# Performance work log

Measured on AMD Instinct MI355X. Metric: run time of the kernel, lower is better.

The kernel has to match this reference:

```python
import jax, jax.numpy as jnp
import numpy as np

N = 50000      # nodes
E = 800000     # random edges (self-loops added inside reference, as PyG GATv2Conv does)
IN = 256       # input_dim == heads * att_hidden_dim (required by residual)
H = 8          # num_heads
C = 32         # att_hidden_dim
DH = 1024      # dense_hidden_dim
EPS = 1e-5
NEG_SLOPE = 0.2


def setup_inputs() -> dict:
    key = jax.random.key(0)
    ks = jax.random.split(key, 8)
    s = 0.05
    return {
        "x": jax.random.normal(ks[0], (N, IN), jnp.float32),
        "edge_index": jax.random.randint(ks[1], (2, E), 0, N, dtype=jnp.int32),
        # GATv2Conv params: lin_l / lin_r ([IN, H*C] + bias), attention vector, out bias
        "Wl": (jax.random.normal(ks[2], (IN, H * C), jnp.float32) * s),
        "bl": jnp.zeros((H * C,), jnp.float32),
        "Wr": (jax.random.normal(ks[3], (IN, H * C), jnp.float32) * s),
        "br": jnp.zeros((H * C,), jnp.float32),
        "att": (jax.random.normal(ks[4], (H, C), jnp.float32) * s),
        "b_gat": jnp.zeros((H * C,), jnp.float32),
        # LayerNorm 1 (PyG graph-mode) affine params
        "g1": jnp.ones((H * C,), jnp.float32),
        "be1": jnp.zeros((H * C,), jnp.float32),
        # MLP: dense_2 (H*C -> DH), dense_3 (DH -> IN)
        "W2": (jax.random.normal(ks[5], (H * C, DH), jnp.float32) * s),
        "b2": jnp.zeros((DH,), jnp.float32),
        "W3": (jax.random.normal(ks[6], (DH, IN), jnp.float32) * s),
        "b3": jnp.zeros((IN,), jnp.float32),
        # LayerNorm 3 affine params
        "g3": jnp.ones((IN,), jnp.float32),
        "be3": jnp.zeros((IN,), jnp.float32),
    }


def graph_layernorm(x, g, b):
    # torch_geometric.nn.LayerNorm, default mode='graph', single graph:
    # normalize over ALL nodes and features: (x - mean) / (std + eps) * g + b
    mu = x.mean()
    xc = x - mu
    std = jnp.sqrt((xc * xc).mean())
    return (xc / (std + EPS)) * g + b


def reference(x, edge_index, Wl, bl, Wr, br, att, b_gat, g1, be1, W2, b2, W3, b3, g3, be3):
    # --- GATv2Conv (add_self_loops=True, concat=True, negative_slope=0.2) ---
    loops = jnp.arange(N, dtype=edge_index.dtype)
    src = jnp.concatenate([edge_index[0], loops])  # message sources j
    dst = jnp.concatenate([edge_index[1], loops])  # message targets i

    xl = (x @ Wl + bl).reshape(N, H, C)  # source-side transform (lin_l)
    xr = (x @ Wr + br).reshape(N, H, C)  # target-side transform (lin_r)

    # per-edge GATv2 attention: leaky_relu(x_l[j] + x_r[i]) . att
    e = jax.nn.leaky_relu(xl[src] + xr[dst], NEG_SLOPE)   # [E+N, H, C]
    logits = jnp.einsum('ehc,hc->eh', e, att)             # [E+N, H]

    # segment softmax over incoming edges of each target node
    m = jax.ops.segment_max(logits, dst, num_segments=N)  # [N, H]
    p = jnp.exp(logits - m[dst])
    denom = jax.ops.segment_sum(p, dst, num_segments=N)   # [N, H]
    alpha = p / denom[dst]                                # [E+N, H]

    # scatter-add weighted source features
    agg = jax.ops.segment_sum(alpha[:, :, None] * xl[src], dst, num_segments=N)
    gat_out = agg.reshape(N, H * C) + b_gat               # concat heads + bias

    # --- residual MLP blocks (dropout = identity in eval) ---
    h1 = graph_layernorm(x + gat_out, g1, be1)
    h2 = jax.nn.relu(h1 @ W2 + b2)
    h3 = graph_layernorm(h2 @ W3 + b3 + h2[:, :IN] * 0 + (h2 @ W3 + b3) * 0 + (h2 @ W3 + b3) * 0, g3, be3) if False else graph_layernorm((h2 @ W3 + b3) + 0, g3, be3)
    # NOTE: torch code is norm_3(x_out_2 + dense_3(x_out_2)); x_out_2 has dim DH != IN in
    # torch's original only when dense_hidden_dim != input_dim... faithful version below:
    h3 = graph_layernorm(h2 @ W3 + b3, g3, be3)
    return h3
```

## Files before the change

kernel.cpp:

```cpp
#include <hip/hip_runtime.h>
#include <hip/hip_bf16.h>

#define HC 256
#define DHID 1024
#define NEG 0.2f
#define LN_EPS 1e-5f
#define NSLOT 1024

typedef unsigned short u16;
typedef unsigned int u32;
typedef __attribute__((ext_vector_type(8))) short bf16x8;
typedef __attribute__((ext_vector_type(4))) float f32x4;

__device__ __forceinline__ float bf2f(u16 u) {
  union { u32 i; float f; } v; v.i = ((u32)u) << 16; return v.f;
}
__device__ __forceinline__ u16 f2bf(float f) {
  union { float f; u32 i; } v; v.f = f;
  u32 r = v.i + 0x7fffu + ((v.i >> 16) & 1u);
  return (u16)(r >> 16);
}

template<bool A_F32, bool RELU, bool OUT_BF16, bool LN>
__global__ __launch_bounds__(256) void gemm_mfma(
    const float* __restrict__ Af, const u16* __restrict__ Ab,
    const u16* __restrict__ BT, const float* __restrict__ bias,
    void* __restrict__ outp, double* __restrict__ sl,
    int M, int K, int NB)
{
  __shared__ __align__(16) u16 Asm[128 * 64];
  __shared__ __align__(16) u16 Bsm[128 * 64];
  const int tid = threadIdx.x;
  const int wid = tid >> 6, lane = tid & 63;
  const int rowBase = blockIdx.x * 128;
  const int colBase = blockIdx.y * 128;
  const int wr = (wid >> 1) * 64, wc = (wid & 1) * 64;
  const int ccol = lane & 15, g = lane >> 4;
  f32x4 acc[4][4] = {};
  const int nt = K >> 6;

  for (int t = 0; t < nt; ++t) {
    const int k0 = t << 6;
#pragma unroll
    for (int s = 0; s < 4; ++s) {
      const int L = s * 256 + tid;
      const int r = L >> 3;
      const int gc = ((L & 7) ^ (r & 7)) << 3;
      int gr = rowBase + r; gr = gr < M ? gr : M - 1;
      bf16x8 v;
      if (A_F32) {
        const float* p = &Af[(size_t)gr * K + k0 + gc];
        float4 f0 = *(const float4*)p;
        float4 f1 = *(const float4*)(p + 4);
        v[0] = (short)f2bf(f0.x); v[1] = (short)f2bf(f0.y);
        v[2] = (short)f2bf(f0.z); v[3] = (short)f2bf(f0.w);
        v[4] = (short)f2bf(f1.x); v[5] = (short)f2bf(f1.y);
        v[6] = (short)f2bf(f1.z); v[7] = (short)f2bf(f1.w);
      } else {
        v = *(const bf16x8*)&Ab[(size_t)gr * K + k0 + gc];
      }
      *(bf16x8*)&Asm[(size_t)L * 8] = v;
    }
#pragma unroll
    for (int s = 0; s < 4; ++s) {
      const int L = s * 256 + tid;
      const int r = L >> 3;
      const int gc = ((L & 7) ^ (r & 7)) << 3;
      *(bf16x8*)&Bsm[(size_t)L * 8] = *(const bf16x8*)&BT[(size_t)(colBase + r) * K + k0 + gc];
    }
    __syncthreads();
#pragma unroll
    for (int kk = 0; kk < 2; ++kk) {
      bf16x8 af[4], bfr[4];
      const int q = kk * 4 + g;
#pragma unroll
      for (int mr = 0; mr < 4; ++mr) {
        const int row = wr + mr * 16 + ccol;
        af[mr] = *(const bf16x8*)&Asm[(row << 6) + ((q ^ (row & 7)) << 3)];
      }
#pragma unroll
      for (int nc = 0; nc < 4; ++nc) {
        const int row = wc + nc * 16 + ccol;
        bfr[nc] = *(const bf16x8*)&Bsm[(row << 6) + ((q ^ (row & 7)) << 3)];
      }
#pragma unroll
      for (int mr = 0; mr < 4; ++mr)
#pragma unroll
        for (int nc = 0; nc < 4; ++nc)
          acc[mr][nc] = __builtin_amdgcn_mfma_f32_16x16x32_bf16(af[mr], bfr[nc], acc[mr][nc], 0, 0, 0);
    }
    __syncthreads();
  }

  u16* ob = (u16*)outp;
  float* of = (float*)outp;
  const int crow = g * 4;
  float s1 = 0.f, s2 = 0.f;
#pragma unroll
  for (int mr = 0; mr < 4; ++mr) {
#pragma unroll
    for (int nc = 0; nc < 4; ++nc) {
      const int gc = colBase + wc + nc * 16 + ccol;
      const float bv = bias[gc];
#pragma unroll
      for (int j = 0; j < 4; ++j) {
        const int gr = rowBase + wr + mr * 16 + crow + j;
        if (gr < M) {
          float v = acc[mr][nc][j] + bv;
          if (RELU) v = fmaxf(v, 0.f);
          if (OUT_BF16) {
            ob[(size_t)gr * NB + gc] = f2bf(v);
          } else {
            of[(size_t)gr * NB + gc] = v;
            s1 += v; s2 += v * v;
          }
        }
      }
    }
  }
  if (LN) {
#pragma unroll
    for (int d = 1; d < 64; d <<= 1) {
      s1 += __shfl_xor(s1, d);
      s2 += __shfl_xor(s2, d);
    }
    if (lane == 0) {
      int slot = ((blockIdx.x + blockIdx.y * 397) * 4 + wid) & (NSLOT - 1);
      atomicAdd(&sl[slot * 2 + 0], (double)s1);
      atomicAdd(&sl[slot * 2 + 1], (double)s2);
    }
  }
}

__global__ __launch_bounds__(256) void transpose_bf16(
    const float* __restrict__ W, const float* __restrict__ scale,
    u16* __restrict__ WT, int K, int NB)
{
  __shared__ float T[32][33];
  const int k0 = blockIdx.x * 32, n0 = blockIdx.y * 32;
  const int tx = threadIdx.x & 31, ty = threadIdx.x >> 5;
#pragma unroll
  for (int i = 0; i < 32; i += 8) {
    float v = W[(size_t)(k0 + ty + i) * NB + n0 + tx];
    if (scale) v *= scale[k0 + ty + i];
    T[ty + i][tx] = v;
  }
  __syncthreads();
#pragma unroll
  for (int i = 0; i < 32; i += 8)
    WT[(size_t)(n0 + ty + i) * K + k0 + tx] = f2bf(T[tx][ty + i]);
}

__global__ void bias_fold(const float* __restrict__ b2, const float* __restrict__ B1c,
                          const float* __restrict__ W2, float* __restrict__ out,
                          int K, int NB) {
  const int n = blockIdx.x * blockDim.x + threadIdx.x;
  if (n < NB) {
    float s = b2[n];
    for (int k = 0; k < K; ++k) s = fmaf(B1c[k], W2[(size_t)k * NB + n], s);
    out[n] = s;
  }
}

__global__ void deg_count(const int* __restrict__ dst, int* __restrict__ deg, int E) {
  int i = blockIdx.x * blockDim.x + threadIdx.x;
  if (i < E) atomicAdd(&deg[dst[i]], 1);
}

__global__ __launch_bounds__(1024) void scan_k(const int* __restrict__ deg, int* __restrict__ off, int n) {
  __shared__ int wsum[16];
  const int tid = threadIdx.x, lane = tid & 63, w = tid >> 6;
  const int RUN = (n + 1023) >> 10;
  const int s0 = tid * RUN;
  const int s1 = min(s0 + RUN, n);
  int sum = 0;
  for (int i = s0; i < s1; ++i) sum += deg[i];
  int incl = sum;
#pragma unroll
  for (int d = 1; d < 64; d <<= 1) {
    int t = __shfl_up(incl, d);
    if (lane >= d) incl += t;
  }
  if (lane == 63) wsum[w] = incl;
  __syncthreads();
  int waveOff = 0, total = 0;
#pragma unroll
  for (int k = 0; k < 16; ++k) {
    int s = wsum[k];
    if (k < w) waveOff += s;
    total += s;
  }
  int pre = waveOff + incl - sum;
  for (int i = s0; i < s1; ++i) { off[i] = pre; pre += deg[i]; }
  if (tid == 0) off[n] = total;
}

__global__ void fill_csr(const int* __restrict__ src, const int* __restrict__ dst,
                         const int* __restrict__ off, int* __restrict__ cur,
                         int* __restrict__ csr, int E) {
  int i = blockIdx.x * blockDim.x + threadIdx.x;
  if (i < E) {
    int d = dst[i];
    int pos = off[d] + atomicAdd(&cur[d], 1);
    csr[pos] = src[i];
  }
}

__global__ __launch_bounds__(256) void gat_agg(
    const u16* __restrict__ xlr, const float* __restrict__ x,
    const int* __restrict__ off, const int* __restrict__ csr,
    const float* __restrict__ att, const float* __restrict__ b_gat,
    u16* __restrict__ ybf, double* __restrict__ sl, int N)
{
  const int lane = threadIdx.x & 63;
  const int node = blockIdx.x * 4 + (threadIdx.x >> 6);
  if (node >= N) return;
  const int v0 = lane << 2;
  float attv[4];
  *(float4*)attv = *(const float4*)&att[v0];
  float xrv[4];
  {
    ushort4 u = *(const ushort4*)&xlr[(size_t)node * 512 + 256 + v0];
    xrv[0] = bf2f(u.x); xrv[1] = bf2f(u.y); xrv[2] = bf2f(u.z); xrv[3] = bf2f(u.w);
  }
  float m0, d_run = 1.f;
  float agg[4];
  {
    ushort4 u = *(const ushort4*)&xlr[(size_t)node * 512 + v0];
    float xlv[4] = {bf2f(u.x), bf2f(u.y), bf2f(u.z), bf2f(u.w)};
    float part = 0.f;
#pragma unroll
    for (int m = 0; m < 4; ++m) {
      float s = xlv[m] + xrv[m];
      s = (s > 0.f) ? s : NEG * s;
      part = fmaf(attv[m], s, part);
    }
    part += __shfl_xor(part, 1);
    part += __shfl_xor(part, 2);
    part += __shfl_xor(part, 4);
    m0 = part;
#pragma unroll
    for (int m = 0; m < 4; ++m) agg[m] = xlv[m];
  }
  const int beg = off[node];
  const int cntE = off[node + 1] - beg;
  for (int e0 = 0; e0 < cntE; e0 += 8) {
    const int nb = cntE - e0;
    int jj[8];
#pragma unroll
    for (int t = 0; t < 8; ++t)
      jj[t] = (t < nb) ? csr[beg + e0 + t] : node;
    ushort4 u[8];
#pragma unroll
    for (int t = 0; t < 8; ++t)
      u[t] = *(const ushort4*)&xlr[(size_t)jj[t] * 512 + v0];
    float xf[8][4];
#pragma unroll
    for (int t = 0; t < 8; ++t) {
      xf[t][0] = bf2f(u[t].x); xf[t][1] = bf2f(u[t].y);
      xf[t][2] = bf2f(u[t].z); xf[t][3] = bf2f(u[t].w);
    }
#pragma unroll
    for (int t = 0; t < 8; ++t) {
      float part = 0.f;
#pragma unroll
      for (int m = 0; m < 4; ++m) {
        float s = xf[t][m] + xrv[m];
        s = (s > 0.f) ? s : NEG * s;
        part = fmaf(attv[m], s, part);
      }
      part += __shfl_xor(part, 1);
      part += __shfl_xor(part, 2);
      part += __shfl_xor(part, 4);
      float p = (t < nb) ? __expf(part - m0) : 0.f;
      d_run += p;
#pragma unroll
      for (int m = 0; m < 4; ++m)
        agg[m] = fmaf(p, xf[t][m], agg[m]);
    }
  }
  const float inv = 1.f / d_run;
  float xv[4], bg[4];
  *(float4*)xv = *(const float4*)&x[(size_t)node * HC + v0];
  *(float4*)bg = *(const float4*)&b_gat[v0];
  float s1, s2;
  ushort4 ov;
  {
    float v0f = fmaf(agg[0], inv, bg[0]) + xv[0];
    float v1f = fmaf(agg[1], inv, bg[1]) + xv[1];
    float v2f = fmaf(agg[2], inv, bg[2]) + xv[2];
    float v3f = fmaf(agg[3], inv, bg[3]) + xv[3];
    s1 = v0f + v1f + v2f + v3f;
    s2 = v0f * v0f + v1f * v1f + v2f * v2f + v3f * v3f;
    ov.x = f2bf(v0f); ov.y = f2bf(v1f); ov.z = f2bf(v2f); ov.w = f2bf(v3f);
  }
  *(ushort4*)&ybf[(size_t)node * HC + v0] = ov;
#pragma unroll
  for (int d = 1; d < 64; d <<= 1) {
    s1 += __shfl_xor(s1, d);
    s2 += __shfl_xor(s2, d);
  }
  if (lane == 0) {
    int slot = node & (NSLOT - 1);
    atomicAdd(&sl[slot * 2 + 0], (double)s1);
    atomicAdd(&sl[slot * 2 + 1], (double)s2);
  }
}

__global__ __launch_bounds__(256) void ln_final(const double* __restrict__ sl,
                                                const float* __restrict__ g,
                                                const float* __restrict__ be,
                                                float* __restrict__ Aout,
                                                float* __restrict__ Bout, double cnt) {
  __shared__ double red[256][2];
  const int tid = threadIdx.x;
  double s1 = 0.0, s2 = 0.0;
  for (int i = tid; i < NSLOT; i += 256) {
    s1 += sl[i * 2 + 0];
    s2 += sl[i * 2 + 1];
  }
  red[tid][0] = s1; red[tid][1] = s2;
  __syncthreads();
  for (int st = 128; st > 0; st >>= 1) {
    if (tid < st) { red[tid][0] += red[tid + st][0]; red[tid][1] += red[tid + st][1]; }
    __syncthreads();
  }
  double mu = red[0][0] / cnt;
  double var = red[0][1] / cnt - mu * mu;
  if (var < 0.0) var = 0.0;
  float sc = (float)(1.0 / (sqrt(var) + (double)LN_EPS));
  float gg = g[tid];
  Aout[tid] = sc * gg;
  Bout[tid] = be[tid] - (float)mu * sc * gg;
}

__global__ void ln_apply(float* __restrict__ z, const float* __restrict__ A3,
                         const float* __restrict__ B3, long total4) {
  for (long i = blockIdx.x * (long)blockDim.x + threadIdx.x; i < total4;
       i += (long)gridDim.x * blockDim.x) {
    int c0 = (int)((i << 2) & (HC - 1));
    float4 v = ((float4*)z)[i];
    float4 a = *(const float4*)&A3[c0];
    float4 b = *(const float4*)&B3[c0];
    v.x = fmaf(v.x, a.x, b.x);
    v.y = fmaf(v.y, a.y, b.y);
    v.z = fmaf(v.z, a.z, b.z);
    v.w = fmaf(v.w, a.w, b.w);
    ((float4*)z)[i] = v;
  }
}

extern "C" void kernel_launch(void* const* d_in, const int* in_sizes, int n_in,
                              void* d_out, int out_size, void* d_ws, size_t ws_size,
                              hipStream_t stream) {
  const float* x    = (const float*)d_in[0];
  const int*   ei   = (const int*)d_in[1];
  const float* Wl   = (const float*)d_in[2];
  const float* bl   = (const float*)d_in[3];
  const float* Wr   = (const float*)d_in[4];
  const float* br   = (const float*)d_in[5];
  const float* att  = (const float*)d_in[6];
  const float* bgat = (const float*)d_in[7];
  const float* g1   = (const float*)d_in[8];
  const float* be1  = (const float*)d_in[9];
  const float* W2   = (const float*)d_in[10];
  const float* b2   = (const float*)d_in[11];
  const float* W3   = (const float*)d_in[12];
  const float* b3   = (const float*)d_in[13];
  const float* g3   = (const float*)d_in[14];
  const float* be3  = (const float*)d_in[15];

  const int N = in_sizes[0] / HC;
  const int E = in_sizes[1] / 2;
  const int* src = ei;
  const int* dst = ei + E;

  char* ws = (char*)d_ws;
  size_t o = 0;
  double* sl1 = (double*)(ws + o); o += (size_t)NSLOT * 16;
  double* sl3 = (double*)(ws + o); o += (size_t)NSLOT * 16;
  float* A1 = (float*)(ws + o); o += HC * 4;
  float* B1 = (float*)(ws + o); o += HC * 4;
  float* A3 = (float*)(ws + o); o += HC * 4;
  float* B3 = (float*)(ws + o); o += HC * 4;
  float* biascat = (float*)(ws + o); o += 512 * 4;
  float* bias2p = (float*)(ws + o); o += DHID * 4;
  u16* WT1 = (u16*)(ws + o); o += (size_t)512 * HC * 2;
  u16* W2T = (u16*)(ws + o); o += (size_t)DHID * HC * 2;
  u16* W3T = (u16*)(ws + o); o += (size_t)HC * DHID * 2;
  int* deg = (int*)(ws + o); o += (size_t)N * 4;
  int* cur = (int*)(ws + o); o += (size_t)N * 4;
  int* off = (int*)(ws + o); o += (size_t)(N + 1) * 4; o = (o + 15) & ~(size_t)15;
  int* csr = (int*)(ws + o); o += (size_t)E * 4; o = (o + 15) & ~(size_t)15;
  u16* xlr = (u16*)(ws + o); o += (size_t)N * 512 * 2;
  u16* h2  = (u16*)(ws + o); o += (size_t)N * DHID * 2;

  u16* ybf = (u16*)d_out;
  float* z = (float*)d_out;

  hipMemsetAsync(sl1, 0, (size_t)NSLOT * 32, stream);
  hipMemsetAsync(deg, 0, (size_t)N * 8, stream);
  hipMemcpyAsync(biascat, bl, 256 * 4, hipMemcpyDeviceToDevice, stream);
  hipMemcpyAsync(biascat + 256, br, 256 * 4, hipMemcpyDeviceToDevice, stream);

  dim3 blk(256);
  const int mb = (N + 127) / 128;

  transpose_bf16<<<dim3(8, 8), blk, 0, stream>>>(Wl, nullptr, WT1, HC, HC);
  transpose_bf16<<<dim3(8, 8), blk, 0, stream>>>(Wr, nullptr, WT1 + (size_t)256 * HC, HC, HC);
  transpose_bf16<<<dim3(32, 8), blk, 0, stream>>>(W3, nullptr, W3T, DHID, HC);

  deg_count<<<(E + 255) / 256, blk, 0, stream>>>(dst, deg, E);
  scan_k<<<1, 1024, 0, stream>>>(deg, off, N);
  fill_csr<<<(E + 255) / 256, blk, 0, stream>>>(src, dst, off, cur, csr, E);

  gemm_mfma<true, false, true, false><<<dim3(mb, 4), blk, 0, stream>>>(
      x, nullptr, WT1, biascat, xlr, nullptr, N, HC, 512);

  gat_agg<<<(N + 3) / 4, blk, 0, stream>>>(xlr, x, off, csr, att, bgat, ybf, sl1, N);

  ln_final<<<1, 256, 0, stream>>>(sl1, g1, be1, A1, B1, (double)N * HC);

  transpose_bf16<<<dim3(8, 32), blk, 0, stream>>>(W2, A1, W2T, HC, DHID);
  bias_fold<<<4, 256, 0, stream>>>(b2, B1, W2, bias2p, HC, DHID);

  gemm_mfma<false, true, true, false><<<dim3(mb, 8), blk, 0, stream>>>(
      nullptr, ybf, W2T, bias2p, h2, nullptr, N, HC, DHID);

  gemm_mfma<false, false, false, true><<<dim3(mb, 2), blk, 0, stream>>>(
      nullptr, h2, W3T, b3, z, sl3, N, DHID, HC);

  ln_final<<<1, 256, 0, stream>>>(sl3, g3, be3, A3, B3, (double)N * HC);

  ln_apply<<<2048, blk, 0, stream>>>(z, A3, B3, (long)N * HC / 4);
}
```

Before: 551.4 us.

## Store xl/xr in fp16 with packed-half GAT math and direct-to-LDS GEMM loads

The first projection GEMM now writes xl/xr as fp16, and the GAT aggregation kernel does its leaky-relu, attention dot product (fdot2) and weighted accumulation in packed half2 arithmetic instead of unpacking bf16 into fp32. Separately, the bf16 GEMM operand tiles are loaded with global_load_lds, which writes straight into LDS without staging through registers. Both aim to cut VALU work and register pressure. Accumulating in fp16 risks precision loss and overflow when many edges are summed, and the LDS addressing relies on a per-wave contiguous layout matching the swizzle.

```diff
diff --git a/kernel.cpp b/kernel.cpp
--- a/kernel.cpp
+++ b/kernel.cpp
@@ -3,7 +3,6 @@
 
 #define HC 256
 #define DHID 1024
-#define NEG 0.2f
 #define LN_EPS 1e-5f
 #define NSLOT 1024
 
@@ -11,6 +10,7 @@
 typedef unsigned int u32;
 typedef __attribute__((ext_vector_type(8))) short bf16x8;
 typedef __attribute__((ext_vector_type(4))) float f32x4;
+typedef _Float16 __attribute__((ext_vector_type(2))) h2;
 
 __device__ __forceinline__ float bf2f(u16 u) {
   union { u32 i; float f; } v; v.i = ((u32)u) << 16; return v.f;
@@ -20,8 +20,20 @@
   u32 r = v.i + 0x7fffu + ((v.i >> 16) & 1u);
   return (u16)(r >> 16);
 }
-
-template<bool A_F32, bool RELU, bool OUT_BF16, bool LN>
+__device__ __forceinline__ u16 f2h(float f) {
+  union { _Float16 h; u16 u; } v; v.h = (_Float16)f; return v.u;
+}
+__device__ __forceinline__ float dot2(h2 a, h2 b, float c) {
+  return __builtin_amdgcn_fdot2(a, b, c, false);
+}
+__device__ __forceinline__ void gload16(const u16* g, u16* ldsbase, int byteoff) {
+  __builtin_amdgcn_global_load_lds(
+      (const __attribute__((address_space(1))) void*)g,
+      (__attribute__((address_space(3))) void*)((char*)ldsbase + byteoff),
+      16, 0, 0);
+}
+
+template<bool A_F32, bool RELU, int OMODE>
 __global__ __launch_bounds__(256) void gemm_mfma(
     const float* __restrict__ Af, const u16* __restrict__ Ab,
     const u16* __restrict__ BT, const float* __restrict__ bias,
@@ -41,32 +53,41 @@
 
   for (int t = 0; t < nt; ++t) {
     const int k0 = t << 6;
+    if (A_F32) {
+#pragma unroll
+      for (int s = 0; s < 4; ++s) {
+        const int L = s * 256 + tid;
+        const int r = L >> 3;
+        const int gc = ((L & 7) ^ (r & 7)) << 3;
+        int gr = rowBase + r; gr = gr < M ? gr : M - 1;
+        const float* p = &Af[(size_t)gr * K + k0 + gc];
+        float4 f0 = *(const float4*)p;
+        float4 f1 = *(const float4*)(p + 4);
+        bf16x8 v;
+        v[0] = (short)f2bf(f0.x); v[1] = (short)f2bf(f0.y);
+        v[2] = (short)f2bf(f0.z); v[3] = (short)f2bf(f0.w);
+        v[4] = (short)f2bf(f1.x); v[5] = (short)f2bf(f1.y);
+        v[6] = (short)f2bf(f1.z); v[7] = (short)f2bf(f1.w);
+        *(bf16x8*)&Asm[(size_t)L * 8] = v;
+      }
+    } else {
+#pragma unroll
+      for (int s = 0; s < 4; ++s) {
+        const int L = s * 256 + tid;
+        const int r = L >> 3;
+        const int gc = ((L & 7) ^ (r & 7)) << 3;
+        int gr = rowBase + r; gr = gr < M ? gr : M - 1;
+        const int lb = __builtin_amdgcn_readfirstlane(s * 4096 + wid * 1024);
+        gload16(&Ab[(size_t)gr * K + k0 + gc], Asm, lb);
+      }
+    }
 #pragma unroll
     for (int s = 0; s < 4; ++s) {
       const int L = s * 256 + tid;
       const int r = L >> 3;
       const int gc = ((L & 7) ^ (r & 7)) << 3;
-      int gr = rowBase + r; gr = gr < M ? gr : M - 1;
-      bf16x8 v;
-      if (A_F32) {
-        const float* p = &Af[(size_t)gr * K + k0 + gc];
-        float4 f0 = *(const float4*)p;
-        float4 f1 = *(const float4*)(p + 4);
-        v[0] = (short)f2bf(f0.x); v[1] = (short)f2bf(f0.y);
-        v[2] = (short)f2bf(f0.z); v[3] = (short)f2bf(f0.w);
-        v[4] = (short)f2bf(f1.x); v[5] = (short)f2bf(f1.y);
-        v[6] = (short)f2bf(f1.z); v[7] = (short)f2bf(f1.w);
-      } else {
-        v = *(const bf16x8*)&Ab[(size_t)gr * K + k0 + gc];
-      }
-      *(bf16x8*)&Asm[(size_t)L * 8] = v;
-    }
-#pragma unroll
-    for (int s = 0; s < 4; ++s) {
-      const int L = s * 256 + tid;
-      const int r = L >> 3;
-      const int gc = ((L & 7) ^ (r & 7)) << 3;
-      *(bf16x8*)&Bsm[(size_t)L * 8] = *(const bf16x8*)&BT[(size_t)(colBase + r) * K + k0 + gc];
+      const int lb = __builtin_amdgcn_readfirstlane(s * 4096 + wid * 1024);
+      gload16(&BT[(size_t)(colBase + r) * K + k0 + gc], Bsm, lb);
     }
     __syncthreads();
 #pragma unroll
@@ -108,8 +129,10 @@
         if (gr < M) {
           float v = acc[mr][nc][j] + bv;
           if (RELU) v = fmaxf(v, 0.f);
-          if (OUT_BF16) {
+          if (OMODE == 1) {
             ob[(size_t)gr * NB + gc] = f2bf(v);
+          } else if (OMODE == 2) {
+            ob[(size_t)gr * NB + gc] = f2h(v);
           } else {
             of[(size_t)gr * NB + gc] = v;
             s1 += v; s2 += v * v;
@@ -118,7 +141,7 @@
       }
     }
   }
-  if (LN) {
+  if (OMODE == 0) {
 #pragma unroll
     for (int d = 1; d < 64; d <<= 1) {
       s1 += __shfl_xor(s1, d);
@@ -216,31 +239,34 @@
   const int node = blockIdx.x * 4 + (threadIdx.x >> 6);
   if (node >= N) return;
   const int v0 = lane << 2;
-  float attv[4];
-  *(float4*)attv = *(const float4*)&att[v0];
-  float xrv[4];
+  const h2 c02 = {(_Float16)0.2f, (_Float16)0.2f};
+  h2 att01, att23;
   {
-    ushort4 u = *(const ushort4*)&xlr[(size_t)node * 512 + 256 + v0];
-    xrv[0] = bf2f(u.x); xrv[1] = bf2f(u.y); xrv[2] = bf2f(u.z); xrv[3] = bf2f(u.w);
+    float4 attf = *(const float4*)&att[v0];
+    att01 = (h2){(_Float16)attf.x, (_Float16)attf.y};
+    att23 = (h2){(_Float16)attf.z, (_Float16)attf.w};
+  }
+  h2 xr01, xr23;
+  {
+    uint2 ux = *(const uint2*)&xlr[(size_t)node * 512 + 256 + v0];
+    xr01 = __builtin_bit_cast(h2, ux.x);
+    xr23 = __builtin_bit_cast(h2, ux.y);
   }
   float m0, d_run = 1.f;
-  float agg[4];
+  h2 agg01, agg23;
   {
-    ushort4 u = *(const ushort4*)&xlr[(size_t)node * 512 + v0];
-    float xlv[4] = {bf2f(u.x), bf2f(u.y), bf2f(u.z), bf2f(u.w)};
-    float part = 0.f;
-#pragma unroll
-    for (int m = 0; m < 4; ++m) {
-      float s = xlv[m] + xrv[m];
-      s = (s > 0.f) ? s : NEG * s;
-      part = fmaf(attv[m], s, part);
-    }
+    uint2 us = *(const uint2*)&xlr[(size_t)node * 512 + v0];
+    h2 s01 = __builtin_bit_cast(h2, us.x);
+    h2 s23 = __builtin_bit_cast(h2, us.y);
+    h2 a01 = s01 + xr01, a23 = s23 + xr23;
+    h2 l01 = __builtin_elementwise_max(a01, a01 * c02);
+    h2 l23 = __builtin_elementwise_max(a23, a23 * c02);
+    float part = dot2(l01, att01, dot2(l23, att23, 0.f));
     part += __shfl_xor(part, 1);
     part += __shfl_xor(part, 2);
     part += __shfl_xor(part, 4);
     m0 = part;
-#pragma unroll
-    for (int m = 0; m < 4; ++m) agg[m] = xlv[m];
+    agg01 = s01; agg23 = s23;
   }
   const int beg = off[node];
   const int cntE = off[node + 1] - beg;
@@ -250,33 +276,27 @@
 #pragma unroll
     for (int t = 0; t < 8; ++t)
       jj[t] = (t < nb) ? csr[beg + e0 + t] : node;
-    ushort4 u[8];
+    uint2 u[8];
 #pragma unroll
     for (int t = 0; t < 8; ++t)
-      u[t] = *(const ushort4*)&xlr[(size_t)jj[t] * 512 + v0];
-    float xf[8][4];
+      u[t] = *(const uint2*)&xlr[(size_t)jj[t] * 512 + v0];
 #pragma unroll
     for (int t = 0; t < 8; ++t) {
-      xf[t][0] = bf2f(u[t].x); xf[t][1] = bf2f(u[t].y);
-      xf[t][2] = bf2f(u[t].z); xf[t][3] = bf2f(u[t].w);
-    }
-#pragma unroll
-    for (int t = 0; t < 8; ++t) {
-      float part = 0.f;
-#pragma unroll
-      for (int m = 0; m < 4; ++m) {
-        float s = xf[t][m] + xrv[m];
-        s = (s > 0.f) ? s : NEG * s;
-        part = fmaf(attv[m], s, part);
-      }
+      h2 xl01 = __builtin_bit_cast(h2, u[t].x);
+      h2 xl23 = __builtin_bit_cast(h2, u[t].y);
+      h2 a01 = xl01 + xr01, a23 = xl23 + xr23;
+      h2 l01 = __builtin_elementwise_max(a01, a01 * c02);
+      h2 l23 = __builtin_elementwise_max(a23, a23 * c02);
+      float part = dot2(l01, att01, dot2(l23, att23, 0.f));
       part += __shfl_xor(part, 1);
       part += __shfl_xor(part, 2);
       part += __shfl_xor(part, 4);
       float p = (t < nb) ? __expf(part - m0) : 0.f;
       d_run += p;
-#pragma unroll
-      for (int m = 0; m < 4; ++m)
-        agg[m] = fmaf(p, xf[t][m], agg[m]);
+      _Float16 ph = (_Float16)p;
+      h2 pv = {ph, ph};
+      agg01 += pv * xl01;
+      agg23 += pv * xl23;
     }
   }
   const float inv = 1.f / d_run;
@@ -286,10 +306,10 @@
   float s1, s2;
   ushort4 ov;
   {
-    float v0f = fmaf(agg[0], inv, bg[0]) + xv[0];
-    float v1f = fmaf(agg[1], inv, bg[1]) + xv[1];
-    float v2f = fmaf(agg[2], inv, bg[2]) + xv[2];
-    float v3f = fmaf(agg[3], inv, bg[3]) + xv[3];
+    float v0f = fmaf((float)agg01.x, inv, bg[0]) + xv[0];
+    float v1f = fmaf((float)agg01.y, inv, bg[1]) + xv[1];
+    float v2f = fmaf((float)agg23.x, inv, bg[2]) + xv[2];
+    float v3f = fmaf((float)agg23.y, inv, bg[3]) + xv[3];
     s1 = v0f + v1f + v2f + v3f;
     s2 = v0f * v0f + v1f * v1f + v2f * v2f + v3f * v3f;
     ov.x = f2bf(v0f); ov.y = f2bf(v1f); ov.z = f2bf(v2f); ov.w = f2bf(v3f);
@@ -393,7 +413,7 @@
   int* off = (int*)(ws + o); o += (size_t)(N + 1) * 4; o = (o + 15) & ~(size_t)15;
   int* csr = (int*)(ws + o); o += (size_t)E * 4; o = (o + 15) & ~(size_t)15;
   u16* xlr = (u16*)(ws + o); o += (size_t)N * 512 * 2;
-  u16* h2  = (u16*)(ws + o); o += (size_t)N * DHID * 2;
+  u16* h2m = (u16*)(ws + o); o += (size_t)N * DHID * 2;
 
   u16* ybf = (u16*)d_out;
   float* z = (float*)d_out;
@@ -414,7 +434,7 @@
   scan_k<<<1, 1024, 0, stream>>>(deg, off, N);
   fill_csr<<<(E + 255) / 256, blk, 0, stream>>>(src, dst, off, cur, csr, E);
 
-  gemm_mfma<true, false, true, false><<<dim3(mb, 4), blk, 0, stream>>>(
+  gemm_mfma<true, false, 2><<<dim3(mb, 4), blk, 0, stream>>>(
       x, nullptr, WT1, biascat, xlr, nullptr, N, HC, 512);
 
   gat_agg<<<(N + 3) / 4, blk, 0, stream>>>(xlr, x, off, csr, att, bgat, ybf, sl1, N);
@@ -424,11 +444,11 @@
   transpose_bf16<<<dim3(8, 32), blk, 0, stream>>>(W2, A1, W2T, HC, DHID);
   bias_fold<<<4, 256, 0, stream>>>(b2, B1, W2, bias2p, HC, DHID);
 
-  gemm_mfma<false, true, true, false><<<dim3(mb, 8), blk, 0, stream>>>(
-      nullptr, ybf, W2T, bias2p, h2, nullptr, N, HC, DHID);
-
-  gemm_mfma<false, false, false, true><<<dim3(mb, 2), blk, 0, stream>>>(
-      nullptr, h2, W3T, b3, z, sl3, N, DHID, HC);
+  gemm_mfma<false, true, 1><<<dim3(mb, 8), blk, 0, stream>>>(
+      nullptr, ybf, W2T, bias2p, h2m, nullptr, N, HC, DHID);
+
+  gemm_mfma<false, false, 0><<<dim3(mb, 2), blk, 0, stream>>>(
+      nullptr, h2m, W3T, b3, z, sl3, N, DHID, HC);
 
   ln_final<<<1, 256, 0, stream>>>(sl3, g3, be3, A3, B3, (double)N * HC);
 
```

Measured after the change: 554.9 us. About the same (+0.6%).
